# Kernel optimization log

Measured on AMD Instinct MI355X. Metric: run time of the kernel, lower is better.

The kernel has to match this reference:

```python
import jax, jax.numpy as jnp
import numpy as np

V, E, B = 40000, 240000, 8
HID, LAT, TDIM, NL = 128, 64, 16, 4

def _w(k, shape):
    fan_in = shape[-2] if len(shape) >= 2 else 1
    return jax.random.normal(k, shape, dtype=jnp.float32) / jnp.sqrt(jnp.float32(fan_in))

def setup_inputs() -> dict:
    key = jax.random.key(0)
    ks = jax.random.split(key, 24)
    inp = {
        'pos': jax.random.normal(ks[0], (V, 3), dtype=jnp.float32),
        't': jax.random.uniform(ks[1], (B,), dtype=jnp.float32),
        'z': jax.random.normal(ks[2], (B, LAT), dtype=jnp.float32),
        'edge_index': jax.random.randint(ks[3], (2, E), 0, V, dtype=jnp.int64),
        'batch': jax.random.randint(ks[4], (V,), 0, B, dtype=jnp.int64),
        # time_embed: Linear(1,16) -> SiLU -> Linear(16,16)
        'te_w1': _w(ks[5], (1, TDIM)), 'te_b1': jnp.zeros((TDIM,), jnp.float32),
        'te_w2': _w(ks[6], (TDIM, TDIM)), 'te_b2': jnp.zeros((TDIM,), jnp.float32),
        # cond_proj: Linear(latent+time, hidden)
        'cp_w': _w(ks[7], (LAT + TDIM, HID)), 'cp_b': jnp.zeros((HID,), jnp.float32),
        # EGNN layers (stacked over n_layers)
        'We1': _w(ks[8], (NL, 2 * HID + 1, HID)), 'be1': jnp.zeros((NL, HID), jnp.float32),
        'We2': _w(ks[9], (NL, HID, HID)), 'be2': jnp.zeros((NL, HID), jnp.float32),
        'Wc1': _w(ks[10], (NL, HID, HID)), 'bc1': jnp.zeros((NL, HID), jnp.float32),
        'Wc2': _w(ks[11], (NL, HID, 1)),
        'Wn1': _w(ks[12], (NL, 2 * HID, HID)), 'bn1': jnp.zeros((NL, HID), jnp.float32),
        'Wn2': _w(ks[13], (NL, HID, HID)), 'bn2': jnp.zeros((NL, HID), jnp.float32),
    }
    return inp

def reference(pos, t, z, edge_index, batch,
              te_w1, te_b1, te_w2, te_b2, cp_w, cp_b,
              We1, be1, We2, be2, Wc1, bc1, Wc2, Wn1, bn1, Wn2, bn2):
    silu = jax.nn.silu
    # conditioning: per-node time embedding + latent code -> h (V, HID)
    t_node = t[batch][:, None]                      # (V,1)
    t_emb = silu(t_node @ te_w1 + te_b1) @ te_w2 + te_b2   # (V, TDIM)
    h = jnp.concatenate([z[batch], t_emb], axis=-1) @ cp_w + cp_b  # (V, HID)

    row, col = edge_index[0], edge_index[1]
    x = pos
    for l in range(NL):
        rel = x[row] - x[col]                       # (E,3)
        d2 = jnp.sum(rel * rel, axis=-1, keepdims=True)  # (E,1)
        e_in = jnp.concatenate([h[row], h[col], d2], axis=-1)  # (E, 2H+1)
        m = silu(silu(e_in @ We1[l] + be1[l]) @ We2[l] + be2[l])  # (E,H)
        coef = silu(m @ Wc1[l] + bc1[l]) @ Wc2[l]   # (E,1)
        x = x + jax.ops.segment_sum(rel * coef, row, num_segments=V)
        agg = jax.ops.segment_sum(m, row, num_segments=V)  # (V,H)
        n_in = jnp.concatenate([h, agg], axis=-1)
        h = h + silu(n_in @ Wn1[l] + bn1[l]) @ Wn2[l] + bn2[l]
    velocity = x - pos
    return velocity
```

## Files before the change

### kernel.cpp

```cpp
#include <hip/hip_runtime.h>

#define HID 128
#define NLAY 4

typedef float f32x4 __attribute__((ext_vector_type(4)));
typedef short bf16x8 __attribute__((ext_vector_type(8)));

union FragU { uint4 u; bf16x8 v; };

__device__ __forceinline__ float silu_f(float x) {
  float e = __expf(-x);
  return x * __builtin_amdgcn_rcpf(1.0f + e);
}

__device__ __forceinline__ unsigned int pack_pair(float x) {
  unsigned int bx = __float_as_uint(x);
  unsigned int hi = bx & 0xffff0000u;
  float lof = x - __uint_as_float(hi);
  return (bx >> 16) | (__float_as_uint(lof) & 0xffff0000u);
}

__device__ __forceinline__ float unpack_sum(unsigned int p) {
  return __uint_as_float(p << 16) + __uint_as_float(p & 0xffff0000u);
}

__device__ __forceinline__ void unpack_frags(const uint4& a, const uint4& b,
                                             FragU& hi, FragU& lo) {
  hi.u.x = __builtin_amdgcn_perm(a.y, a.x, 0x05040100u);
  hi.u.y = __builtin_amdgcn_perm(a.w, a.z, 0x05040100u);
  hi.u.z = __builtin_amdgcn_perm(b.y, b.x, 0x05040100u);
  hi.u.w = __builtin_amdgcn_perm(b.w, b.z, 0x05040100u);
  lo.u.x = __builtin_amdgcn_perm(a.y, a.x, 0x07060302u);
  lo.u.y = __builtin_amdgcn_perm(a.w, a.z, 0x07060302u);
  lo.u.z = __builtin_amdgcn_perm(b.y, b.x, 0x07060302u);
  lo.u.w = __builtin_amdgcn_perm(b.w, b.z, 0x07060302u);
}

__device__ __forceinline__ void pack8(const float* uu, FragU& hi, FragU& lo) {
  unsigned int h[8], l[8];
  #pragma unroll
  for (int i = 0; i < 8; ++i) {
    unsigned int b = __float_as_uint(uu[i]);
    h[i] = b >> 16;
    float lof = uu[i] - __uint_as_float(b & 0xffff0000u);
    l[i] = __float_as_uint(lof) >> 16;
  }
  hi.u.x = h[0] | (h[1] << 16);
  hi.u.y = h[2] | (h[3] << 16);
  hi.u.z = h[4] | (h[5] << 16);
  hi.u.w = h[6] | (h[7] << 16);
  lo.u.x = l[0] | (l[1] << 16);
  lo.u.y = l[2] | (l[3] << 16);
  lo.u.z = l[4] | (l[5] << 16);
  lo.u.w = l[6] | (l[7] << 16);
}

__global__ void wprep_all_kernel(const float* __restrict__ We1, const float* __restrict__ We2,
                                 const float* __restrict__ Wc1, const float* __restrict__ Wn1,
                                 const float* __restrict__ Wn2, unsigned short* __restrict__ wfrag) {
  int gid = blockIdx.x * 256 + threadIdx.x;
  int mat = gid >> 14;
  if (mat >= 28) return;
  int id = gid & 16383;
  int l = mat / 7, j = mat % 7;
  const float* src;
  switch (j) {
    case 0: src = We1 + (size_t)l*257*HID; break;
    case 1: src = We1 + (size_t)l*257*HID + 128*HID; break;
    case 2: src = We2 + (size_t)l*HID*HID; break;
    case 3: src = Wc1 + (size_t)l*HID*HID; break;
    case 4: src = Wn1 + (size_t)l*256*HID; break;
    case 5: src = Wn1 + (size_t)l*256*HID + 128*HID; break;
    default: src = Wn2 + (size_t)l*HID*HID; break;
  }
  unsigned short* out = wfrag + (size_t)mat*32768;
  int i = id & 7;
  int lane = (id >> 3) & 63;
  int obkb = id >> 9;
  int k = (obkb >> 3) * 32 + ((lane >> 4) << 3) + i;
  int col = (obkb & 7) * 16 + (lane & 15);
  float x = src[k * 128 + col];
  unsigned int bx = __float_as_uint(x);
  unsigned int hi = bx & 0xffff0000u;
  float lof = x - __uint_as_float(hi);
  out[id] = (unsigned short)(bx >> 16);
  out[16384 + id] = (unsigned short)(__float_as_uint(lof) >> 16);
}

__global__ void hb_kernel(const float* __restrict__ t, const float* __restrict__ z,
                          const float* __restrict__ te_w1, const float* __restrict__ te_b1,
                          const float* __restrict__ te_w2, const float* __restrict__ te_b2,
                          const float* __restrict__ cp_w, const float* __restrict__ cp_b,
                          float* __restrict__ hb) {
  int b = blockIdx.x;
  int j = threadIdx.x;
  float tv = t[b];
  float e1[16];
  #pragma unroll
  for (int i = 0; i < 16; ++i) e1[i] = silu_f(tv * te_w1[i] + te_b1[i]);
  float acc = cp_b[j];
  for (int i = 0; i < 64; ++i) acc += z[b*64 + i] * cp_w[i*HID + j];
  #pragma unroll
  for (int i = 0; i < 16; ++i) {
    float te = te_b2[i];
    #pragma unroll
    for (int k = 0; k < 16; ++k) te += e1[k] * te_w2[k*16 + i];
    acc += te * cp_w[(64 + i)*HID + j];
  }
  hb[b*HID + j] = acc;
}

__global__ void scatter_h_kernel(const int* __restrict__ batch, const float* __restrict__ hb,
                                 float* __restrict__ h, int V) {
  int idx = blockIdx.x * blockDim.x + threadIdx.x;
  if (idx < V * 32) {
    int v = idx >> 5, c = idx & 31;
    int b = batch[v];
    ((float4*)h)[(size_t)v*32 + c] = ((const float4*)hb)[b*32 + c];
  }
}

__global__ void packx_kernel(const float* __restrict__ pos, float4* __restrict__ x4, int V) {
  int v = blockIdx.x * blockDim.x + threadIdx.x;
  if (v < V) x4[v] = make_float4(pos[3*v], pos[3*v+1], pos[3*v+2], 0.f);
}

__global__ void hist_kernel(const int* __restrict__ rowp, int* __restrict__ cnt, int E) {
  int e = blockIdx.x * blockDim.x + threadIdx.x;
  if (e < E) atomicAdd(&cnt[rowp[e]], 1);
}

__global__ void scan_kernel(const int* __restrict__ cnt, int* __restrict__ offp, int V) {
  __shared__ int s[1024];
  __shared__ int carry_s;
  int tid = threadIdx.x;
  if (tid == 0) carry_s = 0;
  __syncthreads();
  for (int base = 0; base < V; base += 1024) {
    int v = base + tid;
    int val = (v < V) ? cnt[v] : 0;
    s[tid] = val;
    __syncthreads();
    for (int d = 1; d < 1024; d <<= 1) {
      int tval = (tid >= d) ? s[tid - d] : 0;
      __syncthreads();
      s[tid] += tval;
      __syncthreads();
    }
    int c0 = carry_s;
    if (v < V) offp[v] = c0 + s[tid] - val;
    int tot = s[1023];
    __syncthreads();
    if (tid == 0) carry_s = c0 + tot;
    __syncthreads();
  }
  if (tid == 0) offp[V] = carry_s;
}

__global__ void scatter_perm_kernel(const int* __restrict__ rowp, const int* __restrict__ colp,
                                    const int* __restrict__ offp, int* __restrict__ fill,
                                    int* __restrict__ srow, int* __restrict__ scol, int E) {
  int e = blockIdx.x * blockDim.x + threadIdx.x;
  if (e < E) {
    int r = rowp[e];
    int p = offp[r] + atomicAdd(&fill[r], 1);
    srow[p] = r;
    scol[p] = colp[e];
  }
}

template<int MODE>
__global__ __launch_bounds__(512, 2) void ngemm_kernel(
    const float* __restrict__ in, const unsigned short* __restrict__ wfr,
    const float* __restrict__ bias, const float* __restrict__ addsrc,
    float* __restrict__ out, int V)
{
  extern __shared__ uint4 ldsB[];
  for (int i = threadIdx.x; i < 4096; i += 512) ldsB[i] = ((const uint4*)wfr)[i];
  __syncthreads();
  const int tid = threadIdx.x;
  const int wave = tid >> 6, lane = tid & 63;
  const int g = lane >> 4, c16 = lane & 15;
  float bias_r[8];
  if (MODE == 1 || MODE == 3) {
    #pragma unroll
    for (int ob = 0; ob < 8; ++ob) bias_r[ob] = bias[ob*16 + c16];
  }
  const int gw = blockIdx.x*8 + wave;
  const int nw = gridDim.x*8;
  const int ntiles = V >> 5;
  for (int tt = gw; tt < ntiles; tt += nw) {
    int vb = tt << 5;
    int rowA0 = vb + c16, rowA1 = vb + 16 + c16;
    f32x4 zero4 = {0.f, 0.f, 0.f, 0.f};
    f32x4 acc[2][8];
    #pragma unroll
    for (int s = 0; s < 2; ++s)
      #pragma unroll
      for (int ob = 0; ob < 8; ++ob) acc[s][ob] = zero4;
    #pragma unroll
    for (int kb = 0; kb < 4; ++kb) {
      int ch0 = kb*32 + g*8;
      FragU Ah[2], Al[2];
      #pragma unroll
      for (int s = 0; s < 2; ++s) {
        const float4* pr = (const float4*)(in + (size_t)(s ? rowA1 : rowA0)*HID + ch0);
        float4 a0 = pr[0], a1 = pr[1];
        float uu[8] = {a0.x, a0.y, a0.z, a0.w, a1.x, a1.y, a1.z, a1.w};
        pack8(uu, Ah[s], Al[s]);
      }
      #pragma unroll
      for (int ob = 0; ob < 8; ++ob) {
        FragU Bh, Bl;
        Bh.u = ldsB[(kb*8 + ob)*64 + lane];
        Bl.u = ldsB[2048 + (kb*8 + ob)*64 + lane];
        #pragma unroll
        for (int s = 0; s < 2; ++s) {
          acc[s][ob] = __builtin_amdgcn_mfma_f32_16x16x32_bf16(Al[s].v, Bh.v, acc[s][ob], 0, 0, 0);
          acc[s][ob] = __builtin_amdgcn_mfma_f32_16x16x32_bf16(Ah[s].v, Bl.v, acc[s][ob], 0, 0, 0);
          acc[s][ob] = __builtin_amdgcn_mfma_f32_16x16x32_bf16(Ah[s].v, Bh.v, acc[s][ob], 0, 0, 0);
        }
      }
    }
    #pragma unroll
    for (int s = 0; s < 2; ++s)
      #pragma unroll
      for (int ob = 0; ob < 8; ++ob)
        #pragma unroll
        for (int r = 0; r < 4; ++r) {
          int v = vb + s*16 + 4*g + r;
          size_t idx = (size_t)v*HID + ob*16 + c16;
          float val = acc[s][ob][r];
          if (MODE == 0) out[idx] = val;
          if (MODE == 1) out[idx] = val + bias_r[ob];
          if (MODE == 2) out[idx] = silu_f(val + addsrc[idx]);
          if (MODE == 3) out[idx] += val + bias_r[ob];
        }
  }
}

__global__ __launch_bounds__(512, 2) void edge_fused_kernel(
    const int* __restrict__ srow, const int* __restrict__ scol,
    const float4* __restrict__ x4,
    const float* __restrict__ p1, const float* __restrict__ p2,
    const unsigned short* __restrict__ wfrE2, const unsigned short* __restrict__ wfrC1,
    const float* __restrict__ wd2_l, const float* __restrict__ be2_l,
    const float* __restrict__ bc1_l, const float* __restrict__ Wc2_l,
    unsigned int* __restrict__ m_pairs, float4* __restrict__ rc_ws, int E)
{
  extern __shared__ uint4 lds[];
  uint4* ldsB = lds;
  unsigned int* ldsT = (unsigned int*)(lds + 8192);
  for (int i = threadIdx.x; i < 4096; i += 512) ldsB[i] = ((const uint4*)wfrE2)[i];
  for (int i = threadIdx.x; i < 4096; i += 512) ldsB[4096 + i] = ((const uint4*)wfrC1)[i];
  __syncthreads();
  const int tid = threadIdx.x;
  const int wave = tid >> 6, lane = tid & 63;
  const int g = lane >> 4, c16 = lane & 15;
  unsigned int* myT = ldsT + wave*1024;
  float be2_r[8], bc1_r[8], wc2_r[8];
  #pragma unroll
  for (int ob = 0; ob < 8; ++ob) {
    be2_r[ob] = be2_l[ob*16 + c16];
    bc1_r[ob] = bc1_l[ob*16 + c16];
    wc2_r[ob] = Wc2_l[ob*16 + c16];
  }
  const int swz = (c16 & 7) << 2;
  const int gw = blockIdx.x*8 + wave;
  const int nw = gridDim.x*8;
  const int ntiles = E >> 5;
  for (int tt = gw; tt < ntiles; tt += nw) {
    int ib = tt << 5;
    int r_[2], c_[2]; float d2_[2], rlx[2], rly[2], rlz[2];
    #pragma unroll
    for (int s = 0; s < 2; ++s) {
      int i = ib + s*16 + c16;
      r_[s] = srow[i]; c_[s] = scol[i];
      float4 xr = x4[r_[s]], xc = x4[c_[s]];
      rlx[s] = xr.x-xc.x; rly[s] = xr.y-xc.y; rlz[s] = xr.z-xc.z;
      d2_[s] = rlx[s]*rlx[s] + rly[s]*rly[s] + rlz[s]*rlz[s];
    }
    f32x4 zero4 = {0.f, 0.f, 0.f, 0.f};
    f32x4 acc[2][8];
    #pragma unroll
    for (int s = 0; s < 2; ++s)
      #pragma unroll
      for (int ob = 0; ob < 8; ++ob) acc[s][ob] = zero4;
    #pragma unroll
    for (int kb = 0; kb < 4; ++kb) {
      int ch0 = kb*32 + g*8;
      float4 w0 = *(const float4*)(wd2_l + ch0);
      float4 w1 = *(const float4*)(wd2_l + ch0 + 4);
      FragU Ah[2], Al[2];
      #pragma unroll
      for (int s = 0; s < 2; ++s) {
        const float4* pr1 = (const float4*)(p1 + (size_t)r_[s]*HID + ch0);
        const float4* pr2 = (const float4*)(p2 + (size_t)c_[s]*HID + ch0);
        float4 a0 = pr1[0], a1 = pr1[1];
        float4 b0 = pr2[0], b1 = pr2[1];
        float d2 = d2_[s];
        float uu[8];
        uu[0] = silu_f(a0.x + b0.x + d2*w0.x);
        uu[1] = silu_f(a0.y + b0.y + d2*w0.y);
        uu[2] = silu_f(a0.z + b0.z + d2*w0.z);
        uu[3] = silu_f(a0.w + b0.w + d2*w0.w);
        uu[4] = silu_f(a1.x + b1.x + d2*w1.x);
        uu[5] = silu_f(a1.y + b1.y + d2*w1.y);
        uu[6] = silu_f(a1.z + b1.z + d2*w1.z);
        uu[7] = silu_f(a1.w + b1.w + d2*w1.w);
        pack8(uu, Ah[s], Al[s]);
      }
      #pragma unroll
      for (int ob = 0; ob < 8; ++ob) {
        FragU Bh, Bl;
        Bh.u = ldsB[(kb*8 + ob)*64 + lane];
        Bl.u = ldsB[2048 + (kb*8 + ob)*64 + lane];
        #pragma unroll
        for (int s = 0; s < 2; ++s) {
          acc[s][ob] = __builtin_amdgcn_mfma_f32_16x16x32_bf16(Al[s].v, Bh.v, acc[s][ob], 0, 0, 0);
          acc[s][ob] = __builtin_amdgcn_mfma_f32_16x16x32_bf16(Ah[s].v, Bl.v, acc[s][ob], 0, 0, 0);
          acc[s][ob] = __builtin_amdgcn_mfma_f32_16x16x32_bf16(Ah[s].v, Bh.v, acc[s][ob], 0, 0, 0);
        }
      }
    }
    #pragma unroll
    for (int s = 0; s < 2; ++s) {
      f32x4 acc2[8];
      #pragma unroll
      for (int ob = 0; ob < 8; ++ob) acc2[ob] = zero4;
      #pragma unroll
      for (int p = 0; p < 2; ++p) {
        #pragma unroll
        for (int ob4 = 0; ob4 < 4; ++ob4) {
          int ob = p*4 + ob4;
          #pragma unroll
          for (int r = 0; r < 4; ++r) {
            int row = 4*g + r;
            float mval = silu_f(acc[s][ob][r] + be2_r[ob]);
            myT[(row << 6) + ((ob4*16 + c16) ^ ((row & 7) << 2))] = pack_pair(mval);
          }
        }
        unsigned int* gout = m_pairs + (size_t)(ib + s*16)*HID + p*64;
        #pragma unroll
        for (int inst = 0; inst < 4; ++inst) {
          int flat = inst*256 + lane*4;
          int row = flat >> 6, col = flat & 63;
          uint4 vv = *(const uint4*)&myT[(row << 6) + (col ^ ((row & 7) << 2))];
          *(uint4*)(gout + (size_t)row*HID + col) = vv;
        }
        #pragma unroll
        for (int kbl = 0; kbl < 2; ++kbl) {
          int kb = p*2 + kbl;
          int col0 = kbl*32 + g*8;
          uint4 a = *(const uint4*)&myT[(c16 << 6) + (col0 ^ swz)];
          uint4 b = *(const uint4*)&myT[(c16 << 6) + ((col0 + 4) ^ swz)];
          FragU Ah, Al;
          unpack_frags(a, b, Ah, Al);
          #pragma unroll
          for (int ob = 0; ob < 8; ++ob) {
            FragU Bh, Bl;
            Bh.u = ldsB[4096 + (kb*8 + ob)*64 + lane];
            Bl.u = ldsB[6144 + (kb*8 + ob)*64 + lane];
            acc2[ob] = __builtin_amdgcn_mfma_f32_16x16x32_bf16(Al.v, Bh.v, acc2[ob], 0, 0, 0);
            acc2[ob] = __builtin_amdgcn_mfma_f32_16x16x32_bf16(Ah.v, Bl.v, acc2[ob], 0, 0, 0);
            acc2[ob] = __builtin_amdgcn_mfma_f32_16x16x32_bf16(Ah.v, Bh.v, acc2[ob], 0, 0, 0);
          }
        }
      }
      float part[4] = {0.f, 0.f, 0.f, 0.f};
      #pragma unroll
      for (int ob = 0; ob < 8; ++ob)
        #pragma unroll
        for (int r = 0; r < 4; ++r) {
          float tv = silu_f(acc2[ob][r] + bc1_r[ob]);
          part[r] += tv * wc2_r[ob];
        }
      #pragma unroll
      for (int r = 0; r < 4; ++r) {
        #pragma unroll
        for (int m = 1; m < 16; m <<= 1) part[r] += __shfl_xor(part[r], m);
      }
      #pragma unroll
      for (int r = 0; r < 4; ++r) {
        float sx = __shfl(rlx[s], 4*g + r);
        float sy = __shfl(rly[s], 4*g + r);
        float sz = __shfl(rlz[s], 4*g + r);
        if (c16 == 0) {
          float cf = part[r];
          rc_ws[ib + s*16 + 4*g + r] = make_float4(sx*cf, sy*cf, sz*cf, 0.f);
        }
      }
    }
  }
}

__global__ void agg_kernel(const int* __restrict__ offp,
                           const unsigned int* __restrict__ m_pairs,
                           const float4* __restrict__ rc_ws,
                           float* __restrict__ agg, float4* __restrict__ x4, int V)
{
  int wave = threadIdx.x >> 6, lane = threadIdx.x & 63;
  int v = blockIdx.x*4 + wave;
  if (v >= V) return;
  int s = offp[v], e = offp[v+1];
  float acc0 = 0.f, acc1 = 0.f;
  float rx = 0.f, ry = 0.f, rz = 0.f;
  for (int i = s; i < e; ++i) {
    uint2 mv = ((const uint2*)m_pairs)[(size_t)i*64 + lane];
    acc0 += unpack_sum(mv.x);
    acc1 += unpack_sum(mv.y);
    float4 rc = rc_ws[i];
    rx += rc.x; ry += rc.y; rz += rc.z;
  }
  ((float2*)agg)[(size_t)v*64 + lane] = make_float2(acc0, acc1);
  if (lane == 0) {
    float4 xv = x4[v];
    xv.x += rx; xv.y += ry; xv.z += rz;
    x4[v] = xv;
  }
}

__global__ void vel_kernel(const float4* __restrict__ x4, const float* __restrict__ pos,
                           float* __restrict__ out, int V) {
  int v = blockIdx.x * blockDim.x + threadIdx.x;
  if (v < V) {
    float4 xv = x4[v];
    out[3*v]   = xv.x - pos[3*v];
    out[3*v+1] = xv.y - pos[3*v+1];
    out[3*v+2] = xv.z - pos[3*v+2];
  }
}

extern "C" void kernel_launch(void* const* d_in, const int* in_sizes, int n_in,
                              void* d_out, int out_size, void* d_ws, size_t ws_size,
                              hipStream_t stream) {
  const float* pos   = (const float*)d_in[0];
  const float* t     = (const float*)d_in[1];
  const float* z     = (const float*)d_in[2];
  const int*   ei    = (const int*)d_in[3];
  const int*   batch = (const int*)d_in[4];
  const float* te_w1 = (const float*)d_in[5];
  const float* te_b1 = (const float*)d_in[6];
  const float* te_w2 = (const float*)d_in[7];
  const float* te_b2 = (const float*)d_in[8];
  const float* cp_w  = (const float*)d_in[9];
  const float* cp_b  = (const float*)d_in[10];
  const float* We1   = (const float*)d_in[11];
  const float* be1   = (const float*)d_in[12];
  const float* We2   = (const float*)d_in[13];
  const float* be2   = (const float*)d_in[14];
  const float* Wc1   = (const float*)d_in[15];
  const float* bc1   = (const float*)d_in[16];
  const float* Wc2   = (const float*)d_in[17];
  const float* Wn1   = (const float*)d_in[18];
  const float* bn1   = (const float*)d_in[19];
  const float* Wn2   = (const float*)d_in[20];
  const float* bn2   = (const float*)d_in[21];

  const int V = in_sizes[4];
  const int E = in_sizes[3] / 2;
  const int* rowp = ei;
  const int* colp = ei + E;

  char* base = (char*)d_ws;
  size_t off_b = 0;
  auto alloc = [&](size_t bytes) -> char* {
    char* p = base + off_b;
    off_b += (bytes + 255) & ~(size_t)255;
    return p;
  };
  float*  h     = (float*) alloc((size_t)V*HID*4);
  float*  pA    = (float*) alloc((size_t)V*HID*4);
  float*  pB    = (float*) alloc((size_t)V*HID*4);
  float4* x4    = (float4*)alloc((size_t)V*16);
  char*   m_buf = alloc((size_t)E*HID*4);
  float4* rc_ws = (float4*)alloc((size_t)E*16);
  float*  hb    = (float*) alloc(8*HID*4);
  int*    cnt   = (int*)   alloc((size_t)V*4);
  int*    offp  = (int*)   alloc((size_t)(V+1)*4);
  int*    fill  = (int*)   alloc((size_t)V*4);
  int*    srow  = (int*)   alloc((size_t)E*4);
  int*    scol  = (int*)   alloc((size_t)E*4);
  unsigned short* wfrag = (unsigned short*)alloc((size_t)NLAY*7*32768*sizeof(unsigned short));
  (void)ws_size; (void)n_in; (void)out_size;

  unsigned int* m_pairs = (unsigned int*)m_buf;
  float* q_buf = (float*)m_buf;

  auto wf = [&](int l, int j) -> unsigned short* {
    return wfrag + ((size_t)(l*7 + j))*32768;
  };

  const int NLDS = 65536;
  const int FLDS = 163840;
  hipFuncSetAttribute((const void*)ngemm_kernel<0>, hipFuncAttributeMaxDynamicSharedMemorySize, NLDS);
  hipFuncSetAttribute((const void*)ngemm_kernel<1>, hipFuncAttributeMaxDynamicSharedMemorySize, NLDS);
  hipFuncSetAttribute((const void*)ngemm_kernel<2>, hipFuncAttributeMaxDynamicSharedMemorySize, NLDS);
  hipFuncSetAttribute((const void*)ngemm_kernel<3>, hipFuncAttributeMaxDynamicSharedMemorySize, NLDS);
  hipFuncSetAttribute((const void*)edge_fused_kernel, hipFuncAttributeMaxDynamicSharedMemorySize, FLDS);

  hb_kernel<<<8, 128, 0, stream>>>(t, z, te_w1, te_b1, te_w2, te_b2, cp_w, cp_b, hb);
  scatter_h_kernel<<<(V*32 + 255)/256, 256, 0, stream>>>(batch, hb, h, V);
  packx_kernel<<<(V + 255)/256, 256, 0, stream>>>(pos, x4, V);
  hipMemsetAsync(cnt, 0, (size_t)V*4, stream);
  hipMemsetAsync(fill, 0, (size_t)V*4, stream);
  hist_kernel<<<(E + 255)/256, 256, 0, stream>>>(rowp, cnt, E);
  scan_kernel<<<1, 1024, 0, stream>>>(cnt, offp, V);
  scatter_perm_kernel<<<(E + 255)/256, 256, 0, stream>>>(rowp, colp, offp, fill, srow, scol, E);

  wprep_all_kernel<<<28*64, 256, 0, stream>>>(We1, We2, Wc1, Wn1, Wn2, wfrag);

  const int ngrid = ((V >> 5) + 7) / 8;
  const int egrid = 256;

  for (int l = 0; l < NLAY; ++l) {
    const float* wd2_l = We1 + (size_t)l*257*HID + 256*HID;
    const float* Wc2_l = Wc2 + (size_t)l*HID;
    const float* be1_l = be1 + l*HID;
    const float* be2_l = be2 + l*HID;
    const float* bc1_l = bc1 + l*HID;
    const float* bn1_l = bn1 + l*HID;
    const float* bn2_l = bn2 + l*HID;

    ngemm_kernel<1><<<ngrid, 512, NLDS, stream>>>(h, wf(l,0), be1_l, nullptr, pA, V);
    ngemm_kernel<0><<<ngrid, 512, NLDS, stream>>>(h, wf(l,1), nullptr, nullptr, pB, V);
    edge_fused_kernel<<<egrid, 512, FLDS, stream>>>(srow, scol, x4, pA, pB,
                                                    wf(l,2), wf(l,3), wd2_l, be2_l,
                                                    bc1_l, Wc2_l, m_pairs, rc_ws, E);
    agg_kernel<<<(V + 3)/4, 256, 0, stream>>>(offp, m_pairs, rc_ws, pB, x4, V);
    ngemm_kernel<1><<<ngrid, 512, NLDS, stream>>>(h, wf(l,4), bn1_l, nullptr, pA, V);
    ngemm_kernel<2><<<ngrid, 512, NLDS, stream>>>(pB, wf(l,5), nullptr, pA, q_buf, V);
    ngemm_kernel<3><<<ngrid, 512, NLDS, stream>>>(q_buf, wf(l,6), bn2_l, nullptr, h, V);
  }
  vel_kernel<<<(V + 255)/256, 256, 0, stream>>>(x4, pos, (float*)d_out, V);
}
```

Before: 1.228 ms.

## Fuse segment-sum aggregation into edge kernel via atomics on sorted rows

Instead of writing per-edge messages (E×128 packed pairs) and coordinate updates to global memory and reducing them in a separate CSR agg kernel, the edge kernel now sums consecutive same-row values in registers and atomically adds them into a zeroed per-node aggregate and a dx buffer. A small kernel then adds dx to positions. This removes the large E×HID write and re-read, at the cost of many float atomics, two memsets per layer, and a summation order that is no longer deterministic.

```diff
diff --git a/kernel.cpp b/kernel.cpp
--- a/kernel.cpp
+++ b/kernel.cpp
@@ -18,10 +18,6 @@
   unsigned int hi = bx & 0xffff0000u;
   float lof = x - __uint_as_float(hi);
   return (bx >> 16) | (__float_as_uint(lof) & 0xffff0000u);
-}
-
-__device__ __forceinline__ float unpack_sum(unsigned int p) {
-  return __uint_as_float(p << 16) + __uint_as_float(p & 0xffff0000u);
 }
 
 __device__ __forceinline__ void unpack_frags(const uint4& a, const uint4& b,
@@ -246,7 +242,7 @@
     const unsigned short* __restrict__ wfrE2, const unsigned short* __restrict__ wfrC1,
     const float* __restrict__ wd2_l, const float* __restrict__ be2_l,
     const float* __restrict__ bc1_l, const float* __restrict__ Wc2_l,
-    unsigned int* __restrict__ m_pairs, float4* __restrict__ rc_ws, int E)
+    float* __restrict__ aggb, float* __restrict__ dx, int E)
 {
   extern __shared__ uint4 lds[];
   uint4* ldsB = lds;
@@ -280,6 +276,12 @@
       rlx[s] = xr.x-xc.x; rly[s] = xr.y-xc.y; rlz[s] = xr.z-xc.z;
       d2_[s] = rlx[s]*rlx[s] + rly[s]*rly[s] + rlz[s]*rlz[s];
     }
+    int rowv[2][4];
+    #pragma unroll
+    for (int s = 0; s < 2; ++s)
+      #pragma unroll
+      for (int r = 0; r < 4; ++r)
+        rowv[s][r] = __shfl(r_[s], 4*g + r);
     f32x4 zero4 = {0.f, 0.f, 0.f, 0.f};
     f32x4 acc[2][8];
     #pragma unroll
@@ -333,20 +335,26 @@
         #pragma unroll
         for (int ob4 = 0; ob4 < 4; ++ob4) {
           int ob = p*4 + ob4;
+          float mv[4];
           #pragma unroll
           for (int r = 0; r < 4; ++r) {
             int row = 4*g + r;
             float mval = silu_f(acc[s][ob][r] + be2_r[ob]);
+            mv[r] = mval;
             myT[(row << 6) + ((ob4*16 + c16) ^ ((row & 7) << 2))] = pack_pair(mval);
           }
-        }
-        unsigned int* gout = m_pairs + (size_t)(ib + s*16)*HID + p*64;
-        #pragma unroll
-        for (int inst = 0; inst < 4; ++inst) {
-          int flat = inst*256 + lane*4;
-          int row = flat >> 6, col = flat & 63;
-          uint4 vv = *(const uint4*)&myT[(row << 6) + (col ^ ((row & 7) << 2))];
-          *(uint4*)(gout + (size_t)row*HID + col) = vv;
+          int cur = rowv[s][0];
+          float sum = mv[0];
+          #pragma unroll
+          for (int r = 1; r < 4; ++r) {
+            int rv = rowv[s][r];
+            if (rv == cur) sum += mv[r];
+            else {
+              atomicAdd(&aggb[(size_t)cur*HID + ob*16 + c16], sum);
+              cur = rv; sum = mv[r];
+            }
+          }
+          atomicAdd(&aggb[(size_t)cur*HID + ob*16 + c16], sum);
         }
         #pragma unroll
         for (int kbl = 0; kbl < 2; ++kbl) {
@@ -380,42 +388,43 @@
         #pragma unroll
         for (int m = 1; m < 16; m <<= 1) part[r] += __shfl_xor(part[r], m);
       }
+      float cxv[4], cyv[4], czv[4];
       #pragma unroll
       for (int r = 0; r < 4; ++r) {
         float sx = __shfl(rlx[s], 4*g + r);
         float sy = __shfl(rly[s], 4*g + r);
         float sz = __shfl(rlz[s], 4*g + r);
-        if (c16 == 0) {
-          float cf = part[r];
-          rc_ws[ib + s*16 + 4*g + r] = make_float4(sx*cf, sy*cf, sz*cf, 0.f);
-        }
+        cxv[r] = sx*part[r]; cyv[r] = sy*part[r]; czv[r] = sz*part[r];
+      }
+      if (c16 == 0) {
+        int cur = rowv[s][0];
+        float ax = cxv[0], ay = cyv[0], az = czv[0];
+        #pragma unroll
+        for (int r = 1; r < 4; ++r) {
+          int rv = rowv[s][r];
+          if (rv == cur) { ax += cxv[r]; ay += cyv[r]; az += czv[r]; }
+          else {
+            atomicAdd(&dx[(size_t)cur*4 + 0], ax);
+            atomicAdd(&dx[(size_t)cur*4 + 1], ay);
+            atomicAdd(&dx[(size_t)cur*4 + 2], az);
+            cur = rv; ax = cxv[r]; ay = cyv[r]; az = czv[r];
+          }
+        }
+        atomicAdd(&dx[(size_t)cur*4 + 0], ax);
+        atomicAdd(&dx[(size_t)cur*4 + 1], ay);
+        atomicAdd(&dx[(size_t)cur*4 + 2], az);
       }
     }
   }
 }
 
-__global__ void agg_kernel(const int* __restrict__ offp,
-                           const unsigned int* __restrict__ m_pairs,
-                           const float4* __restrict__ rc_ws,
-                           float* __restrict__ agg, float4* __restrict__ x4, int V)
-{
-  int wave = threadIdx.x >> 6, lane = threadIdx.x & 63;
-  int v = blockIdx.x*4 + wave;
-  if (v >= V) return;
-  int s = offp[v], e = offp[v+1];
-  float acc0 = 0.f, acc1 = 0.f;
-  float rx = 0.f, ry = 0.f, rz = 0.f;
-  for (int i = s; i < e; ++i) {
-    uint2 mv = ((const uint2*)m_pairs)[(size_t)i*64 + lane];
-    acc0 += unpack_sum(mv.x);
-    acc1 += unpack_sum(mv.y);
-    float4 rc = rc_ws[i];
-    rx += rc.x; ry += rc.y; rz += rc.z;
-  }
-  ((float2*)agg)[(size_t)v*64 + lane] = make_float2(acc0, acc1);
-  if (lane == 0) {
+__global__ void adddx_kernel(const float* __restrict__ dx, float4* __restrict__ x4, int V) {
+  int v = blockIdx.x * blockDim.x + threadIdx.x;
+  if (v < V) {
     float4 xv = x4[v];
-    xv.x += rx; xv.y += ry; xv.z += rz;
+    xv.x += dx[(size_t)v*4 + 0];
+    xv.y += dx[(size_t)v*4 + 1];
+    xv.z += dx[(size_t)v*4 + 2];
     x4[v] = xv;
   }
 }
@@ -472,9 +481,10 @@
   float*  h     = (float*) alloc((size_t)V*HID*4);
   float*  pA    = (float*) alloc((size_t)V*HID*4);
   float*  pB    = (float*) alloc((size_t)V*HID*4);
+  float*  aggb  = (float*) alloc((size_t)V*HID*4);
+  float*  q_buf = (float*) alloc((size_t)V*HID*4);
   float4* x4    = (float4*)alloc((size_t)V*16);
-  char*   m_buf = alloc((size_t)E*HID*4);
-  float4* rc_ws = (float4*)alloc((size_t)E*16);
+  float*  dx    = (float*) alloc((size_t)V*16);
   float*  hb    = (float*) alloc(8*HID*4);
   int*    cnt   = (int*)   alloc((size_t)V*4);
   int*    offp  = (int*)   alloc((size_t)(V+1)*4);
@@ -484,9 +494,6 @@
   unsigned short* wfrag = (unsigned short*)alloc((size_t)NLAY*7*32768*sizeof(unsigned short));
   (void)ws_size; (void)n_in; (void)out_size;
 
-  unsigned int* m_pairs = (unsigned int*)m_buf;
-  float* q_buf = (float*)m_buf;
-
   auto wf = [&](int l, int j) -> unsigned short* {
     return wfrag + ((size_t)(l*7 + j))*32768;
   };
@@ -524,12 +531,14 @@
 
     ngemm_kernel<1><<<ngrid, 512, NLDS, stream>>>(h, wf(l,0), be1_l, nullptr, pA, V);
     ngemm_kernel<0><<<ngrid, 512, NLDS, stream>>>(h, wf(l,1), nullptr, nullptr, pB, V);
+    hipMemsetAsync(aggb, 0, (size_t)V*HID*4, stream);
+    hipMemsetAsync(dx, 0, (size_t)V*16, stream);
     edge_fused_kernel<<<egrid, 512, FLDS, stream>>>(srow, scol, x4, pA, pB,
                                                     wf(l,2), wf(l,3), wd2_l, be2_l,
-                                                    bc1_l, Wc2_l, m_pairs, rc_ws, E);
-    agg_kernel<<<(V + 3)/4, 256, 0, stream>>>(offp, m_pairs, rc_ws, pB, x4, V);
+                                                    bc1_l, Wc2_l, aggb, dx, E);
+    adddx_kernel<<<(V + 255)/256, 256, 0, stream>>>(dx, x4, V);
     ngemm_kernel<1><<<ngrid, 512, NLDS, stream>>>(h, wf(l,4), bn1_l, nullptr, pA, V);
-    ngemm_kernel<2><<<ngrid, 512, NLDS, stream>>>(pB, wf(l,5), nullptr, pA, q_buf, V);
+    ngemm_kernel<2><<<ngrid, 512, NLDS, stream>>>(aggb, wf(l,5), nullptr, pA, q_buf, V);
     ngemm_kernel<3><<<ngrid, 512, NLDS, stream>>>(q_buf, wf(l,6), bn2_l, nullptr, h, V);
   }
   vel_kernel<<<(V + 255)/256, 256, 0, stream>>>(x4, pos, (float*)d_out, V);
```

Result: slower. 1.316 ms (+7.2%).
